# Performance work log

Hardware: AMD Instinct MI355X
Metric: run time of the kernel (lower is better)

Reference implementation:

```python
import jax, jax.numpy as jnp
import numpy as np

B, S, H = 64, 256, 768          # batch, seq, feature_size
A = 8                            # atten_num (heads)
GNUM, GSZ = 8192, 64             # group_num, labels per group
LABELS = GNUM * GSZ              # 524288
E = 256                          # args.hidden_size (label embed dim)
TOPK = 10                        # candidates_topk


def setup_inputs() -> dict:
    key = jax.random.key(0)
    ks = jax.random.split(key, 6)
    sc = lambda d: 1.0 / np.sqrt(d)
    return {
        "inputs": jax.random.normal(ks[0], (B, S, H), jnp.float32),
        "W_att": jax.random.normal(ks[1], (A, H), jnp.float32) * sc(H),
        "b_att": jnp.zeros((A,), jnp.float32),
        "W_clf": jax.random.normal(ks[2], (GNUM, H), jnp.float32) * sc(H),
        "b_clf": jnp.zeros((GNUM,), jnp.float32),
        "W_enc": jax.random.normal(ks[3], (E, H), jnp.float32) * sc(H),
        "b_enc": jnp.zeros((E,), jnp.float32),
        "embed_table": jax.random.normal(ks[4], (LABELS, E), jnp.float32) * sc(E),
        "group_y": jnp.arange(LABELS, dtype=jnp.int32).reshape(GNUM, GSZ),
    }


def reference(inputs, W_att, b_att, W_clf, b_clf, W_enc, b_enc, embed_table, group_y):
    # MulitAttention: [B,S,H] -> atten [B,A,S] -> softmax over S -> out [B,A,H]
    atten = jnp.einsum("bsh,ah->bas", inputs, W_att) + b_att[None, :, None]
    atten_sm = jax.nn.softmax(atten, axis=-1)
    out = jnp.einsum("bas,bsh->bah", atten_sm, inputs)

    # group classifier + MaxPool1d over heads -> c_out [B, GNUM]
    group_logits = jnp.einsum("bah,gh->bag", out, W_clf) + b_clf
    c_out = jnp.max(group_logits, axis=1)

    # get_candidates (inference path): sigmoid on detached logits, topk groups,
    # gather group members (fixed group size -> regular [B, TOPK*GSZ])
    probs = jax.nn.sigmoid(jax.lax.stop_gradient(c_out))
    scores, indices = jax.lax.top_k(probs, TOPK)            # [B, TOPK]
    candidates = group_y[indices].reshape(B, TOPK * GSZ)    # [B, C]
    group_candidates_scores = jnp.repeat(scores, GSZ, axis=1)  # [B, C]

    # label scoring: encoder(out) [B,A,E], embed gather [B,C,E],
    # batched dot products [B,A,C], maxpool over heads -> l_out [B,C]
    emb = jnp.einsum("bah,eh->bae", out, W_enc) + b_enc
    embed_weights = embed_table[candidates]                 # [B, C, E]
    logits = jnp.einsum("bce,bae->bac", embed_weights, emb)
    l_out = jnp.max(logits, axis=1)

    return c_out, l_out, candidates, group_candidates_scores
```

## Files before the change

kernel.cpp:

```cpp
#include <hip/hip_runtime.h>

#define B_    64
#define S_    256
#define H_    768
#define A_    8
#define GNUM_ 8192
#define GSZ_  64
#define E_    256
#define TOPK_ 10
#define C_    (TOPK_*GSZ_)
#define BROWS (GNUM_ + E_)

typedef short  bf16x8 __attribute__((ext_vector_type(8)));
typedef float  f32x4  __attribute__((ext_vector_type(4)));

__device__ __forceinline__ ushort f2bf(float x) {
    union { float f; unsigned u; } c; c.f = x;
    unsigned r = c.u + 0x7fff + ((c.u >> 16) & 1);
    return (ushort)(r >> 16);
}
__device__ __forceinline__ float bf2f(ushort h) {
    union { float f; unsigned u; } c; c.u = ((unsigned)h) << 16;
    return c.f;
}
__device__ __forceinline__ float asf(unsigned u) {
    union { unsigned u; float f; } c; c.u = u; return c.f;
}
__device__ __forceinline__ unsigned cvt_pk_bf16(float a, float b) {
    unsigned r;
    asm("v_cvt_pk_bf16_f32 %0, %1, %2" : "=v"(r) : "v"(a), "v"(b));
    return r;
}

__global__ __launch_bounds__(256) void attn1_kernel(
    const float* __restrict__ x, const float* __restrict__ Watt,
    const float* __restrict__ batt, float* __restrict__ attT)
{
    const int b  = blockIdx.x;
    const int s0 = blockIdx.y * 64;
    const int t  = threadIdx.x;
    const int sl = t & 63;
    const int g  = __builtin_amdgcn_readfirstlane(t >> 6);
    __shared__ float Xt[64][65];
    __shared__ float Pp[8][64][5];

    const float* xb = x + ((size_t)b * S_ + s0) * H_;
    float acc[A_] = {};
    int pr[4], pc[4];
    float4 pref[4];
#pragma unroll
    for (int i = 0; i < 4; i++) {
        int fid = i * 256 + t;
        pr[i] = fid >> 4; pc[i] = (fid & 15) * 4;
    }
#pragma unroll
    for (int i = 0; i < 4; i++)
        pref[i] = *(const float4*)(xb + (size_t)pr[i] * H_ + pc[i]);
    for (int h0 = 0; h0 < H_; h0 += 64) {
        __syncthreads();
#pragma unroll
        for (int i = 0; i < 4; i++) {
            float4 v = pref[i];
            float* dst = &Xt[pr[i]][pc[i]];
            dst[0] = v.x; dst[1] = v.y; dst[2] = v.z; dst[3] = v.w;
        }
        __syncthreads();
        if (h0 + 64 < H_) {
#pragma unroll
            for (int i = 0; i < 4; i++)
                pref[i] = *(const float4*)(xb + (size_t)pr[i] * H_ + h0 + 64 + pc[i]);
        }
        const float* wp = Watt + h0 + g * 16;
#pragma unroll
        for (int h = 0; h < 16; h++) {
            float xv = Xt[sl][g * 16 + h];
#pragma unroll
            for (int a = 0; a < A_; a++) acc[a] += xv * wp[a * H_ + h];
        }
    }
#pragma unroll
    for (int a = 0; a < A_; a++) Pp[a][sl][g] = acc[a];
    __syncthreads();
#pragma unroll
    for (int i = 0; i < 2; i++) {
        int idx = i * 256 + t;
        int a = idx >> 6, s2 = idx & 63;
        float v = Pp[a][s2][0] + Pp[a][s2][1] + Pp[a][s2][2] + Pp[a][s2][3] + batt[a];
        attT[(size_t)b * (S_*A_) + (size_t)(s0 + s2) * A_ + a] = v;
    }
}

__global__ __launch_bounds__(384) void attn2s_kernel(
    const float* __restrict__ x, const float* __restrict__ attT,
    ushort* __restrict__ Ah, ushort* __restrict__ Al)
{
    const int b = blockIdx.x, h0 = blockIdx.y * 192, t = threadIdx.x;
    __shared__ float La[S_ * A_];
    __shared__ float Wm[A_][260];
    __shared__ float Cb[A_][192];

    for (int i = t; i < 512; i += 384)
        *(float4*)&La[i * 4] =
            *(const float4*)(attT + (size_t)b * (S_*A_) + (size_t)i * 4);
    __syncthreads();
    if (t < 256) {
        const int a = t >> 5, l = t & 31;
        float mx = -1e30f;
#pragma unroll
        for (int k = 0; k < 8; k++) mx = fmaxf(mx, La[(l + 32*k) * A_ + a]);
#pragma unroll
        for (int off = 16; off >= 1; off >>= 1) mx = fmaxf(mx, __shfl_xor(mx, off));
        float ev[8]; float sm = 0.f;
#pragma unroll
        for (int k = 0; k < 8; k++) { ev[k] = expf(La[(l + 32*k) * A_ + a] - mx); sm += ev[k]; }
#pragma unroll
        for (int off = 16; off >= 1; off >>= 1) sm += __shfl_xor(sm, off);
        float inv = 1.f / sm;
#pragma unroll
        for (int k = 0; k < 8; k++) Wm[a][l + 32*k] = ev[k] * inv;
    }
    __syncthreads();

    const int half = (t >= 192) ? 1 : 0;
    const int col  = t - half * 192;
    const int sbase = half * 128;
    const float* xb = x + (size_t)b * S_ * H_ + (size_t)sbase * H_ + h0 + col;
    float o[A_] = {};
    float xb0[16], xb1[16];
#define LOADSTRIP(buf, ks) { _Pragma("unroll") \
    for (int i = 0; i < 16; i++) buf[i] = xb[(size_t)((ks)*16 + i) * H_]; }
#define COMPSTRIP(buf, ks) { _Pragma("unroll") \
    for (int sg = 0; sg < 4; sg++) { _Pragma("unroll") \
        for (int a = 0; a < A_; a++) { \
            float4 w2 = *(const float4*)&Wm[a][sbase + (ks)*16 + sg*4]; \
            o[a] += w2.x*buf[sg*4+0] + w2.y*buf[sg*4+1] \
                  + w2.z*buf[sg*4+2] + w2.w*buf[sg*4+3]; } } }
    LOADSTRIP(xb0, 0)
#pragma unroll
    for (int kp = 0; kp < 4; kp++) {
        LOADSTRIP(xb1, 2*kp + 1)
        COMPSTRIP(xb0, 2*kp)
        if (kp < 3) LOADSTRIP(xb0, 2*kp + 2)
        COMPSTRIP(xb1, 2*kp + 1)
    }
#undef LOADSTRIP
#undef COMPSTRIP
    if (half == 1) {
#pragma unroll
        for (int a = 0; a < A_; a++) Cb[a][col] = o[a];
    }
    __syncthreads();
    if (half == 0) {
#pragma unroll
        for (int a = 0; a < A_; a++) {
            float v = o[a] + Cb[a][col];
            ushort hi = f2bf(v);
            ushort lo = f2bf(v - bf2f(hi));
            size_t off = (size_t)(b * 8 + a) * H_ + h0 + col;
            Ah[off] = hi; Al[off] = lo;
        }
    }
}

__global__ __launch_bounds__(256, 1) void gemm_mfma_kernel(
    const ushort* __restrict__ Ah, const ushort* __restrict__ Al,
    const float* __restrict__ Wclf, const float* __restrict__ Wenc,
    const float* __restrict__ bclf, const float* __restrict__ benc,
    float* __restrict__ c_out, float* __restrict__ emb)
{
    const int f = blockIdx.x;
    int p, m;
    if (f < 256) {
        const int xcd = f & 7, s = f >> 3;
        p = xcd + 8 * (s >> 2);
        m = s & 3;
    } else {
        const int j = f - 256;
        p = 64 + (j >> 2);
        m = j & 3;
    }
    const int n0 = p * 128, m0 = m * 128;

    __shared__ __align__(16) ushort lds[2][4][128 * 32];
    const int t = threadIdx.x;
    const int w = t >> 6, l = t & 63;
    const int mq = (w & 1) * 64, nq = (w >> 1) * 64;

    const int srow = t >> 2, skc = t & 3;
    const int wr_idx = ((srow * 32 + skc * 8) ^ ((srow & 7) << 3));
    const ushort* baseAh = Ah + (size_t)m0 * H_;
    const ushort* baseAl = Al + (size_t)m0 * H_;
    const float*  baseB  = (n0 < GNUM_) ? (Wclf + (size_t)n0 * H_)
                                        : (Wenc + (size_t)(n0 - GNUM_) * H_);

    uint4  stA[2][2];
    float4 stB[2][2];
    auto loadk = [&](int k0) {
        size_t oA = (size_t)srow * H_ + k0 + skc * 8;
        stA[0][0] = *(const uint4*)(baseAh + oA);
        stA[0][1] = *(const uint4*)(baseAh + oA + (size_t)64 * H_);
        stA[1][0] = *(const uint4*)(baseAl + oA);
        stA[1][1] = *(const uint4*)(baseAl + oA + (size_t)64 * H_);
        const float* bp0 = baseB + (size_t)srow * H_ + k0 + skc * 8;
        const float* bp1 = bp0 + (size_t)64 * H_;
        stB[0][0] = *(const float4*)(bp0);
        stB[0][1] = *(const float4*)(bp0 + 4);
        stB[1][0] = *(const float4*)(bp1);
        stB[1][1] = *(const float4*)(bp1 + 4);
    };

    f32x4 acc[4][4] = {};
    loadk(0);
    const int kc = l >> 4, lr = l & 15;

    for (int kt = 0; kt < H_ / 32; ++kt) {
        ushort* bufp = &lds[kt & 1][0][0];
#pragma unroll
        for (int xx = 0; xx < 2; xx++) {
            *(uint4*)(bufp + xx * 4096 + wr_idx)        = stA[xx][0];
            *(uint4*)(bufp + xx * 4096 + 2048 + wr_idx) = stA[xx][1];
        }
#pragma unroll
        for (int rp = 0; rp < 2; rp++) {
            float fv[8] = { stB[rp][0].x, stB[rp][0].y, stB[rp][0].z, stB[rp][0].w,
                            stB[rp][1].x, stB[rp][1].y, stB[rp][1].z, stB[rp][1].w };
            uint4 hi, lo;
            unsigned* hip = (unsigned*)&hi;
            unsigned* lop = (unsigned*)&lo;
#pragma unroll
            for (int j = 0; j < 4; j++) {
                unsigned pk = cvt_pk_bf16(fv[2*j], fv[2*j+1]);
                hip[j] = pk;
                float r0 = fv[2*j]   - asf(pk << 16);
                float r1 = fv[2*j+1] - asf(pk & 0xffff0000u);
                lop[j] = cvt_pk_bf16(r0, r1);
            }
            *(uint4*)(bufp + 2 * 4096 + rp * 2048 + wr_idx) = hi;
            *(uint4*)(bufp + 3 * 4096 + rp * 2048 + wr_idx) = lo;
        }
        __syncthreads();
        if (kt + 1 < H_ / 32) loadk((kt + 1) * 32);

        bf16x8 fah[4], fal[4], fbh[4], fbl[4];
#pragma unroll
        for (int mt = 0; mt < 4; mt++) {
            int r = mq + mt * 16 + lr;
            int idx = ((r * 32 + kc * 8) ^ ((r & 7) << 3));
            fah[mt] = *(const bf16x8*)(bufp + idx);
            fal[mt] = *(const bf16x8*)(bufp + 4096 + idx);
        }
#pragma unroll
        for (int nt = 0; nt < 4; nt++) {
            int r = nq + nt * 16 + lr;
            int idx = ((r * 32 + kc * 8) ^ ((r & 7) << 3));
            fbh[nt] = *(const bf16x8*)(bufp + 2 * 4096 + idx);
            fbl[nt] = *(const bf16x8*)(bufp + 3 * 4096 + idx);
        }
#pragma unroll
        for (int mt = 0; mt < 4; mt++)
#pragma unroll
            for (int nt = 0; nt < 4; nt++) {
                acc[mt][nt] = __builtin_amdgcn_mfma_f32_16x16x32_bf16(fah[mt], fbh[nt], acc[mt][nt], 0, 0, 0);
                acc[mt][nt] = __builtin_amdgcn_mfma_f32_16x16x32_bf16(fal[mt], fbh[nt], acc[mt][nt], 0, 0, 0);
                acc[mt][nt] = __builtin_amdgcn_mfma_f32_16x16x32_bf16(fah[mt], fbl[nt], acc[mt][nt], 0, 0, 0);
            }
    }

    const int q = l >> 4;
    if (n0 < GNUM_) {
#pragma unroll
        for (int mt = 0; mt < 4; mt++)
#pragma unroll
            for (int nt = 0; nt < 4; nt++) {
                f32x4 a = acc[mt][nt];
                float v = fmaxf(fmaxf(a[0], a[1]), fmaxf(a[2], a[3]));
                v = fmaxf(v, __shfl_xor(v, 16));
                if ((q & 1) == 0) {
                    int mg = m0 + mq + mt * 16 + (q >> 1) * 8;
                    int n  = n0 + nq + nt * 16 + lr;
                    c_out[(size_t)(mg >> 3) * GNUM_ + n] = v + bclf[n];
                }
            }
    } else {
#pragma unroll
        for (int mt = 0; mt < 4; mt++)
#pragma unroll
            for (int nt = 0; nt < 4; nt++) {
                int n = n0 - GNUM_ + nq + nt * 16 + lr;
                float bn = benc[n];
#pragma unroll
                for (int r2 = 0; r2 < 4; r2++) {
                    int mg = m0 + mq + mt * 16 + q * 4 + r2;
                    emb[(size_t)mg * E_ + n] = acc[mt][nt][r2] + bn;
                }
            }
    }
}

__global__ __launch_bounds__(256) void scoretop_kernel(
    const float* __restrict__ c_out, const int* __restrict__ gy,
    const float* __restrict__ embw, const float* __restrict__ et,
    float* __restrict__ l_out, float* __restrict__ cand_f,
    float* __restrict__ gcs)
{
    const int b = blockIdx.x >> 3, q8 = blockIdx.x & 7, t = threadIdx.x;
    __shared__ float el[A_ * E_];
    __shared__ float bvv[4]; __shared__ int bii[4];
    __shared__ float topv[TOPK_]; __shared__ int topi[TOPK_];

#pragma unroll
    for (int i = 0; i < 2; i++) {
        int fid = i * 256 + t;
        *(float4*)&el[fid * 4] = *(const float4*)(embw + (size_t)b * (A_*E_) + fid * 4);
    }

    const float* row = c_out + (size_t)b * GNUM_;
    float lv[TOPK_]; int li[TOPK_];
#pragma unroll
    for (int k = 0; k < TOPK_; k++) { lv[k] = -1.f; li[k] = 0x7fffffff; }
    for (int i = t; i < GNUM_; i += 256) {
        float p = 1.f / (1.f + expf(-row[i]));
        if (p > lv[TOPK_ - 1]) {
            float cv = p; int ci = i;
#pragma unroll
            for (int k = 0; k < TOPK_; k++) {
                bool sw = (cv > lv[k]);
                float tv = sw ? lv[k] : cv; int ti = sw ? li[k] : ci;
                lv[k] = sw ? cv : lv[k];    li[k] = sw ? ci : li[k];
                cv = tv; ci = ti;
            }
        }
    }
    const int lane = t & 63, wv = t >> 6;
    for (int rnd = 0; rnd < TOPK_; rnd++) {
        float bv = lv[0]; int bi = li[0];
#pragma unroll
        for (int off = 32; off >= 1; off >>= 1) {
            float ov = __shfl_xor(bv, off); int oi = __shfl_xor(bi, off);
            if (ov > bv || (ov == bv && oi < bi)) { bv = ov; bi = oi; }
        }
        if (lane == 0) { bvv[wv] = bv; bii[wv] = bi; }
        __syncthreads();
        float gbv = bvv[0]; int gbi = bii[0];
#pragma unroll
        for (int w2 = 1; w2 < 4; w2++) {
            float ov = bvv[w2]; int oi = bii[w2];
            if (ov > gbv || (ov == gbv && oi < gbi)) { gbv = ov; gbi = oi; }
        }
        if (t == 0) { topv[rnd] = gbv; topi[rnd] = gbi; }
        if (li[0] == gbi) {
#pragma unroll
            for (int k = 0; k < TOPK_ - 1; k++) { lv[k] = lv[k + 1]; li[k] = li[k + 1]; }
            lv[TOPK_ - 1] = -1.f; li[TOPK_ - 1] = 0x7fffffff;
        }
        __syncthreads();
    }

    if (q8 == 0) {
        for (int j = t; j < C_; j += 256) {
            int k = j >> 6, slot = j & 63;
            int lbl = gy[topi[k] * GSZ_ + slot];
            cand_f[(size_t)b * C_ + j] = (float)lbl;
            gcs[(size_t)b * C_ + j] = topv[k];
        }
    }

    const int qq = lane >> 4, sub = lane & 15;
    const int cbase = q8 * 80;
    int c0 = cbase + wv * 4 + qq;
    int lbl0 = gy[topi[c0 >> 6] * GSZ_ + (c0 & 63)];
    const float* er = et + (size_t)lbl0 * E_ + sub * 4;
    float4 v0 = *(const float4*)(er);
    float4 v1 = *(const float4*)(er + 64);
    float4 v2 = *(const float4*)(er + 128);
    float4 v3 = *(const float4*)(er + 192);
    for (int pass = 0; pass < 5; pass++) {
        float4 p0, p1, p2, p3;
        if (pass + 1 < 5) {
            int cn = cbase + (pass + 1) * 16 + wv * 4 + qq;
            int lbln = gy[topi[cn >> 6] * GSZ_ + (cn & 63)];
            const float* ern = et + (size_t)lbln * E_ + sub * 4;
            p0 = *(const float4*)(ern);
            p1 = *(const float4*)(ern + 64);
            p2 = *(const float4*)(ern + 128);
            p3 = *(const float4*)(ern + 192);
        }
        float best = -1e30f;
#pragma unroll
        for (int a = 0; a < A_; a++) {
            const float* ep = el + a * E_ + sub * 4;
            float4 w0 = *(const float4*)(ep);
            float4 w1 = *(const float4*)(ep + 64);
            float4 w2 = *(const float4*)(ep + 128);
            float4 w3 = *(const float4*)(ep + 192);
            float pp = v0.x*w0.x + v0.y*w0.y + v0.z*w0.z + v0.w*w0.w
                     + v1.x*w1.x + v1.y*w1.y + v1.z*w1.z + v1.w*w1.w
                     + v2.x*w2.x + v2.y*w2.y + v2.z*w2.z + v2.w*w2.w
                     + v3.x*w3.x + v3.y*w3.y + v3.z*w3.z + v3.w*w3.w;
#pragma unroll
            for (int off = 8; off >= 1; off >>= 1) pp += __shfl_xor(pp, off);
            best = fmaxf(best, pp);
        }
        if (sub == 0) l_out[(size_t)b * C_ + cbase + pass * 16 + wv * 4 + qq] = best;
        v0 = p0; v1 = p1; v2 = p2; v3 = p3;
    }
}

extern "C" void kernel_launch(void* const* d_in, const int* in_sizes, int n_in,
                              void* d_out, int out_size, void* d_ws, size_t ws_size,
                              hipStream_t stream)
{
    (void)in_sizes; (void)n_in; (void)out_size; (void)ws_size;
    const float* x    = (const float*)d_in[0];
    const float* Watt = (const float*)d_in[1];
    const float* batt = (const float*)d_in[2];
    const float* Wclf = (const float*)d_in[3];
    const float* bclf = (const float*)d_in[4];
    const float* Wenc = (const float*)d_in[5];
    const float* benc = (const float*)d_in[6];
    const float* et   = (const float*)d_in[7];
    const int*   gy   = (const int*)d_in[8];

    float* out    = (float*)d_out;
    float* c_out  = out;
    float* l_out  = out + (size_t)B_ * GNUM_;
    float* cand_f = l_out + (size_t)B_ * C_;
    float* gcs    = cand_f + (size_t)B_ * C_;

    char* ws = (char*)d_ws;
    float*  attT = (float*) (ws);
    float*  embw = (float*) (ws + 524288);
    ushort* Ahw  = (ushort*)(ws + 1048576);
    ushort* Alw  = (ushort*)(ws + 1835008);

    attn1_kernel<<<dim3(B_, 4), 256, 0, stream>>>(x, Watt, batt, attT);
    attn2s_kernel<<<dim3(B_, 4), 384, 0, stream>>>(x, attT, Ahw, Alw);
    gemm_mfma_kernel<<<264, 256, 0, stream>>>(Ahw, Alw, Wclf, Wenc, bclf, benc,
                                              c_out, embw);
    scoretop_kernel<<<512, 256, 0, stream>>>(c_out, gy, embw, et,
                                             l_out, cand_f, gcs);
}
```

Measured before the change: 133.7 us.

## Fuse attention-score and softmax-weighted-sum kernels into one, recomputing scores per block

Merges the two attention kernels into a single kernel that computes the per-batch attention scores in shared memory, applies softmax, and produces the weighted sums, removing the intermediate global buffer and one launch. Each of the 3 column blocks per batch recomputes the full 256x8 score matrix redundantly, so it trades extra reads of the input and extra FMAs for fewer launches. The score phase uses only half the 512 threads for compute and drops the register prefetch, and the grid shrinks to 192 blocks.

```diff
diff --git a/kernel.cpp b/kernel.cpp
--- a/kernel.cpp
+++ b/kernel.cpp
@@ -32,77 +32,60 @@
     return r;
 }
 
-__global__ __launch_bounds__(256) void attn1_kernel(
+__global__ __launch_bounds__(512) void attnfused_kernel(
     const float* __restrict__ x, const float* __restrict__ Watt,
-    const float* __restrict__ batt, float* __restrict__ attT)
+    const float* __restrict__ batt,
+    ushort* __restrict__ Ah, ushort* __restrict__ Al)
 {
-    const int b  = blockIdx.x;
-    const int s0 = blockIdx.y * 64;
-    const int t  = threadIdx.x;
-    const int sl = t & 63;
-    const int g  = __builtin_amdgcn_readfirstlane(t >> 6);
+    const int b = blockIdx.x, h0 = blockIdx.y * 256, t = threadIdx.x;
     __shared__ float Xt[64][65];
     __shared__ float Pp[8][64][5];
-
-    const float* xb = x + ((size_t)b * S_ + s0) * H_;
-    float acc[A_] = {};
-    int pr[4], pc[4];
-    float4 pref[4];
-#pragma unroll
-    for (int i = 0; i < 4; i++) {
-        int fid = i * 256 + t;
-        pr[i] = fid >> 4; pc[i] = (fid & 15) * 4;
-    }
-#pragma unroll
-    for (int i = 0; i < 4; i++)
-        pref[i] = *(const float4*)(xb + (size_t)pr[i] * H_ + pc[i]);
-    for (int h0 = 0; h0 < H_; h0 += 64) {
-        __syncthreads();
-#pragma unroll
-        for (int i = 0; i < 4; i++) {
-            float4 v = pref[i];
-            float* dst = &Xt[pr[i]][pc[i]];
-            dst[0] = v.x; dst[1] = v.y; dst[2] = v.z; dst[3] = v.w;
-        }
-        __syncthreads();
-        if (h0 + 64 < H_) {
-#pragma unroll
-            for (int i = 0; i < 4; i++)
-                pref[i] = *(const float4*)(xb + (size_t)pr[i] * H_ + h0 + 64 + pc[i]);
-        }
-        const float* wp = Watt + h0 + g * 16;
-#pragma unroll
-        for (int h = 0; h < 16; h++) {
-            float xv = Xt[sl][g * 16 + h];
-#pragma unroll
-            for (int a = 0; a < A_; a++) acc[a] += xv * wp[a * H_ + h];
-        }
-    }
-#pragma unroll
-    for (int a = 0; a < A_; a++) Pp[a][sl][g] = acc[a];
-    __syncthreads();
-#pragma unroll
-    for (int i = 0; i < 2; i++) {
-        int idx = i * 256 + t;
-        int a = idx >> 6, s2 = idx & 63;
-        float v = Pp[a][s2][0] + Pp[a][s2][1] + Pp[a][s2][2] + Pp[a][s2][3] + batt[a];
-        attT[(size_t)b * (S_*A_) + (size_t)(s0 + s2) * A_ + a] = v;
-    }
-}
-
-__global__ __launch_bounds__(384) void attn2s_kernel(
-    const float* __restrict__ x, const float* __restrict__ attT,
-    ushort* __restrict__ Ah, ushort* __restrict__ Al)
-{
-    const int b = blockIdx.x, h0 = blockIdx.y * 192, t = threadIdx.x;
     __shared__ float La[S_ * A_];
     __shared__ float Wm[A_][260];
-    __shared__ float Cb[A_][192];
-
-    for (int i = t; i < 512; i += 384)
-        *(float4*)&La[i * 4] =
-            *(const float4*)(attT + (size_t)b * (S_*A_) + (size_t)i * 4);
+    __shared__ float Cb[A_][256];
+
+    const float* xbase = x + (size_t)b * S_ * H_;
+
+    for (int sc = 0; sc < 4; sc++) {
+        const float* xb = xbase + (size_t)(sc * 64) * H_;
+        float acc[A_] = {};
+        for (int hc = 0; hc < H_; hc += 64) {
+            __syncthreads();
+#pragma unroll
+            for (int i = 0; i < 2; i++) {
+                int fid = i * 512 + t;
+                int r = fid >> 4, c = (fid & 15) * 4;
+                float4 v = *(const float4*)(xb + (size_t)r * H_ + hc + c);
+                Xt[r][c] = v.x; Xt[r][c+1] = v.y; Xt[r][c+2] = v.z; Xt[r][c+3] = v.w;
+            }
+            __syncthreads();
+            if (t < 256) {
+                const int sl = t & 63, g = t >> 6;
+                const float* wp = Watt + hc + g * 16;
+#pragma unroll
+                for (int h = 0; h < 16; h++) {
+                    float xv = Xt[sl][g * 16 + h];
+#pragma unroll
+                    for (int a = 0; a < A_; a++) acc[a] += xv * wp[a * H_ + h];
+                }
+            }
+        }
+        __syncthreads();
+        if (t < 256) {
+            const int sl = t & 63, g = t >> 6;
+#pragma unroll
+            for (int a = 0; a < A_; a++) Pp[a][sl][g] = acc[a];
+        }
+        __syncthreads();
+        {
+            int a = t >> 6, s2 = t & 63;
+            float v = Pp[a][s2][0] + Pp[a][s2][1] + Pp[a][s2][2] + Pp[a][s2][3]
+                    + batt[a];
+            La[(sc * 64 + s2) * A_ + a] = v;
+        }
+    }
     __syncthreads();
+
     if (t < 256) {
         const int a = t >> 5, l = t & 31;
         float mx = -1e30f;
@@ -121,14 +104,13 @@
     }
     __syncthreads();
 
-    const int half = (t >= 192) ? 1 : 0;
-    const int col  = t - half * 192;
+    const int col = t & 255, half = t >> 8;
     const int sbase = half * 128;
-    const float* xb = x + (size_t)b * S_ * H_ + (size_t)sbase * H_ + h0 + col;
+    const float* xb2 = x + (size_t)b * S_ * H_ + (size_t)sbase * H_ + h0 + col;
     float o[A_] = {};
     float xb0[16], xb1[16];
 #define LOADSTRIP(buf, ks) { _Pragma("unroll") \
-    for (int i = 0; i < 16; i++) buf[i] = xb[(size_t)((ks)*16 + i) * H_]; }
+    for (int i = 0; i < 16; i++) buf[i] = xb2[(size_t)((ks)*16 + i) * H_]; }
 #define COMPSTRIP(buf, ks) { _Pragma("unroll") \
     for (int sg = 0; sg < 4; sg++) { _Pragma("unroll") \
         for (int a = 0; a < A_; a++) { \
@@ -428,13 +410,11 @@
     float* gcs    = cand_f + (size_t)B_ * C_;
 
     char* ws = (char*)d_ws;
-    float*  attT = (float*) (ws);
-    float*  embw = (float*) (ws + 524288);
-    ushort* Ahw  = (ushort*)(ws + 1048576);
-    ushort* Alw  = (ushort*)(ws + 1835008);
-
-    attn1_kernel<<<dim3(B_, 4), 256, 0, stream>>>(x, Watt, batt, attT);
-    attn2s_kernel<<<dim3(B_, 4), 384, 0, stream>>>(x, attT, Ahw, Alw);
+    float*  embw = (float*) (ws);
+    ushort* Ahw  = (ushort*)(ws + 524288);
+    ushort* Alw  = (ushort*)(ws + 1310720);
+
+    attnfused_kernel<<<dim3(B_, 3), 512, 0, stream>>>(x, Watt, batt, Ahw, Alw);
     gemm_mfma_kernel<<<264, 256, 0, stream>>>(Ahw, Alw, Wclf, Wenc, bclf, benc,
                                               c_out, embw);
     scoretop_kernel<<<512, 256, 0, stream>>>(c_out, gy, embw, et,
```

Result: slower. 191.0 us (+42.9%).
